# Optimization experiments

Measured on AMD Instinct MI355X. Metric: run time of the kernel, lower is better.

## Reference

```python
import jax, jax.numpy as jnp
import numpy as np

B, S, D = 4, 2048, 1024
H = 16
HD = D // H  # head dim = 64


def setup_inputs() -> dict:
    key = jax.random.key(0)
    ks = jax.random.split(key, 9)
    s = 1.0 / np.sqrt(D)
    return {
        "Q": jax.random.normal(ks[0], (B, S, D), dtype=jnp.float32),
        "K": jax.random.normal(ks[1], (B, S, D), dtype=jnp.float32),
        "V": jax.random.normal(ks[2], (B, S, D), dtype=jnp.float32),
        "Wq": jax.random.uniform(ks[3], (D, D), jnp.float32, -s, s),
        "bq": jax.random.uniform(ks[4], (D,), jnp.float32, -s, s),
        "Wk": jax.random.uniform(ks[5], (D, D), jnp.float32, -s, s),
        "bk": jax.random.uniform(ks[6], (D,), jnp.float32, -s, s),
        "Wv": jax.random.uniform(ks[7], (D, D), jnp.float32, -s, s),
        "bv": jax.random.uniform(ks[8], (D,), jnp.float32, -s, s),
    }


def reference(Q, K, V, Wq, bq, Wk, bk, Wv, bv):
    # Linear projections, split into heads: (B, H, S, HD)
    def proj(x, W, b):
        y = x @ W + b  # torch Linear uses x @ W.T; here W is stored pre-transposed (D_in, D_out)
        return y.reshape(B, S, H, HD).transpose(0, 2, 1, 3)

    q = proj(Q, Wq, bq)
    k = proj(K, Wk, bk)
    v = proj(V, Wv, bv)

    scale = 1.0 / jnp.sqrt(jnp.float32(HD))
    scores = jnp.einsum("bhqd,bhkd->bhqk", q, k) * scale  # (B,H,S,S)
    # causal mask (mask=True path): -inf above the diagonal
    causal = jnp.triu(jnp.full((S, S), -jnp.inf, dtype=scores.dtype), k=1)
    scores = scores + causal
    attn = jax.nn.softmax(scores, axis=-1)
    ctx = jnp.einsum("bhqk,bhkd->bhqd", attn, v)  # (B,H,S,HD)
    return ctx.transpose(0, 2, 1, 3).reshape(B, S, H * HD)
```

## Files before the change

kernel.cpp:

```cpp
#include <hip/hip_runtime.h>
#include <hip/hip_bf16.h>
#include <stdint.h>

#define B_  4
#define S_  2048
#define D_  1024
#define H_  16
#define HD_ 64
#define LOG2E 1.44269504088896f

typedef unsigned short u16;
typedef short bf16x8 __attribute__((ext_vector_type(8)));
typedef float f32x4 __attribute__((ext_vector_type(4)));

static __device__ __forceinline__ u16 f2bf(float f) {
    union { float f; uint32_t u; } v; v.f = f;
    return (u16)((v.u + 0x7FFF + ((v.u >> 16) & 1)) >> 16);
}

static __device__ __forceinline__ uint32_t cvt_pk_bf16(float lo, float hi) {
    uint32_t r;
    asm("v_cvt_pk_bf16_f32 %0, %1, %2" : "=v"(r) : "v"(lo), "v"(hi));
    return r;
}

static __device__ __forceinline__ uint32_t pk2(float lo, float hi) {
    return __builtin_amdgcn_perm(__float_as_uint(hi), __float_as_uint(lo), 0x07060302u);
}

static __device__ __forceinline__ bf16x8 rd_swz(const u16* base, int row, int slot) {
    return *(const bf16x8*)((const char*)base + row * 128 + ((slot ^ (row & 7)) << 4));
}

static __device__ __forceinline__ void gll_swz(const u16* grow0, size_t stride,
                                               u16* lds_chunk, int lane) {
    const int r = lane >> 3;
    const int slot = (lane & 7) ^ r;
    const u16* g = grow0 + (size_t)r * stride + slot * 8;
    __builtin_amdgcn_global_load_lds(
        (const __attribute__((address_space(1))) uint32_t*)g,
        (__attribute__((address_space(3))) uint32_t*)lds_chunk, 16, 0, 0);
}

__global__ __launch_bounds__(256) void wtrans(
    const float* __restrict__ W0, const float* __restrict__ W1, const float* __restrict__ W2,
    u16* __restrict__ T0, u16* __restrict__ T1, u16* __restrict__ T2)
{
    const float* W = blockIdx.z == 0 ? W0 : (blockIdx.z == 1 ? W1 : W2);
    u16* T       = blockIdx.z == 0 ? T0 : (blockIdx.z == 1 ? T1 : T2);
    __shared__ float t[32][33];
    const int n0 = blockIdx.x * 32, k0 = blockIdx.y * 32;
    const int tx = threadIdx.x, ty = threadIdx.y;
#pragma unroll
    for (int i = 0; i < 4; ++i)
        t[ty + i * 8][tx] = W[(size_t)(k0 + ty + i * 8) * D_ + n0 + tx];
    __syncthreads();
#pragma unroll
    for (int i = 0; i < 4; ++i)
        T[(size_t)(n0 + ty + i * 8) * D_ + k0 + tx] = f2bf(t[tx][ty + i * 8]);
}

template <int MODE>
__global__ __launch_bounds__(256) void proj_gemm(
    const float* __restrict__ X, const u16* __restrict__ Wt,
    const float* __restrict__ bias, u16* __restrict__ out)
{
    __shared__ __align__(16) u16 lA[2][128 * 64];
    __shared__ __align__(16) u16 lB[2][128 * 64];
    const int tid = threadIdx.x;
    const int m0 = blockIdx.x * 128, n0 = blockIdx.y * 128;
    const int w = tid >> 6, lane = tid & 63;
    const int lr = lane & 15, lg = lane >> 4;
    const int wr = (w >> 1) * 64, wc = (w & 1) * 64;

    f32x4 acc[4][4] = {};
    float4 areg[8];

    auto loadA = [&](int k0) {
#pragma unroll
        for (int i = 0; i < 8; ++i) {
            const int lin = i * 1024 + tid * 4;
            const int r = lin >> 6, c = lin & 63;
            areg[i] = *(const float4*)(X + (size_t)(m0 + r) * D_ + k0 + c);
        }
    };
    auto writeA = [&](u16* dst) {
#pragma unroll
        for (int i = 0; i < 8; ++i) {
            const int lin = i * 1024 + tid * 4;
            const int r = lin >> 6, c = lin & 63;
            uint2 pk;
            pk.x = pk2(areg[i].x, areg[i].y);
            pk.y = pk2(areg[i].z, areg[i].w);
            const int phys = r * 128 + (((c >> 3) ^ (r & 7)) << 4) + ((c & 7) << 1);
            *(uint2*)((char*)dst + phys) = pk;
        }
    };
    auto stageB = [&](int k0, u16* dst) {
#pragma unroll
        for (int i = 0; i < 4; ++i) {
            const int c = w * 4 + i;
            gll_swz(Wt + (size_t)(n0 + c * 8) * D_ + k0, D_, dst + c * 512, lane);
        }
    };
    auto mfmaStep = [&](const u16* A, const u16* Bb) {
#pragma unroll
        for (int kk = 0; kk < 2; ++kk) {
            bf16x8 af[4], bfr[4];
#pragma unroll
            for (int m = 0; m < 4; ++m)
                af[m] = rd_swz(A, wr + m * 16 + lr, kk * 4 + lg);
#pragma unroll
            for (int n = 0; n < 4; ++n)
                bfr[n] = rd_swz(Bb, wc + n * 16 + lr, kk * 4 + lg);
#pragma unroll
            for (int m = 0; m < 4; ++m)
#pragma unroll
                for (int n = 0; n < 4; ++n)
                    acc[m][n] = __builtin_amdgcn_mfma_f32_16x16x32_bf16(af[m], bfr[n], acc[m][n], 0, 0, 0);
        }
    };

    loadA(0);
    stageB(0, lB[0]);
    writeA(lA[0]);
    __syncthreads();

    for (int k0 = 0, s = 0; k0 < D_; k0 += 64, s ^= 1) {
        const int nk = k0 + 64;
        if (nk < D_) {
            loadA(nk);
            stageB(nk, lB[s ^ 1]);
        }
        mfmaStep(lA[s], lB[s]);
        if (nk < D_) writeA(lA[s ^ 1]);
        __syncthreads();
    }

#pragma unroll
    for (int m = 0; m < 4; ++m)
#pragma unroll
        for (int n = 0; n < 4; ++n)
#pragma unroll
            for (int j = 0; j < 4; ++j) {
                const int gm = m0 + wr + m * 16 + lg * 4 + j;
                const int gn = n0 + wc + n * 16 + lr;
                float y = acc[m][n][j] + bias[gn];
                if (MODE == 0) y *= 0.125f * LOG2E;
                const int bb = gm >> 11, s2 = gm & (S_ - 1);
                const int h = gn >> 6, hd = gn & 63;
                size_t off;
                if (MODE < 2) off = (((size_t)bb * H_ + h) * S_ + s2) * HD_ + hd;
                else {
                    const int s6 = s2 & 63;
                    const int sp = (s2 & ~63) | (s6 & 0x20) | ((s6 & 0xC) << 1) |
                                   ((s6 & 0x10) >> 2) | (s6 & 3);
                    off = (((size_t)bb * H_ + h) * HD_ + hd) * S_ + sp;
                }
                out[off] = f2bf(y);
            }
}

__global__ __launch_bounds__(512) void attn_kernel(
    const u16* __restrict__ qb, const u16* __restrict__ kb,
    const u16* __restrict__ vtb, float* __restrict__ out)
{
    const int bx = blockIdx.x;
    const int bh = bx & 63;
    const int pi = bx >> 6;
    const int b = bh >> 4, h = bh & 15;
    const int tid = threadIdx.x;
    const int w = tid >> 6, lane = tid & 63;
    const int lr = lane & 15, lg = lane >> 4;

    __shared__ __align__(16) u16 lds[2][4][64 * 64];

    const size_t kbase = (size_t)bh * S_ * HD_;
    const size_t vbase = (size_t)bh * HD_ * S_;

    union { uint32_t u[4]; bf16x8 v; } onesf;
    onesf.u[0] = onesf.u[1] = onesf.u[2] = onesf.u[3] = 0x3F803F80u;

    for (int e = 0; e < 2; ++e) {
        const int qi = e ? (7 - pi) : pi;
        const int q0 = qi * 256;
        const int qrb = q0 + w * 32;

        bf16x8 qf0[2], qf1[2];
#pragma unroll
        for (int s = 0; s < 2; ++s) {
            const size_t qoff = ((size_t)bh * S_ + qrb + s * 16 + lr) * HD_;
            qf0[s] = *(const bf16x8*)(qb + qoff + lg * 8);
            qf1[s] = *(const bf16x8*)(qb + qoff + 32 + lg * 8);
        }

        f32x4 oacc[2][4] = {};
        f32x4 lacc[2] = {};
        const int tmax = 4 * qi + 3;

        auto stage = [&](int tp, int set) {
            const int kvA = tp * 64, kvB = kvA + 64;
            u16* d = &lds[set][0][0];
            gll_swz(kb + kbase + (size_t)(kvA + w * 8) * HD_, HD_, d + w * 512, lane);
            gll_swz(vtb + vbase + (size_t)(w * 8) * S_ + kvA, S_, d + 4096 + w * 512, lane);
            gll_swz(kb + kbase + (size_t)(kvB + w * 8) * HD_, HD_, d + 8192 + w * 512, lane);
            gll_swz(vtb + vbase + (size_t)(w * 8) * S_ + kvB, S_, d + 12288 + w * 512, lane);
        };

        auto compute = [&](int t, const u16* lK, const u16* lV) {
            const int kv0 = t * 64;
            if (kv0 > qrb + 31) return;
            const bool a0 = (kv0 <= qrb + 15);

            f32x4 sacc[2][4];
            __builtin_amdgcn_s_setprio(1);
#pragma unroll
            for (int n = 0; n < 4; ++n) {
                const bf16x8 k0f = rd_swz(lK, n * 16 + lr, lg);
                const bf16x8 k1f = rd_swz(lK, n * 16 + lr, 4 + lg);
                f32x4 z1 = {};
                z1 = __builtin_amdgcn_mfma_f32_16x16x32_bf16(k0f, qf0[1], z1, 0, 0, 0);
                z1 = __builtin_amdgcn_mfma_f32_16x16x32_bf16(k1f, qf1[1], z1, 0, 0, 0);
                sacc[1][n] = z1;
                if (a0) {
                    f32x4 z0 = {};
                    z0 = __builtin_amdgcn_mfma_f32_16x16x32_bf16(k0f, qf0[0], z0, 0, 0, 0);
                    z0 = __builtin_amdgcn_mfma_f32_16x16x32_bf16(k1f, qf1[0], z0, 0, 0, 0);
                    sacc[0][n] = z0;
                }
            }
            __builtin_amdgcn_s_setprio(0);

            if (t >= tmax - 3) {
#pragma unroll
                for (int s = 0; s < 2; ++s)
#pragma unroll
                    for (int n = 0; n < 4; ++n)
#pragma unroll
                        for (int j = 0; j < 4; ++j)
                            if (kv0 + n * 16 + lg * 4 + j > qrb + s * 16 + lr)
                                sacc[s][n][j] = -1e30f;
            }

            union { uint32_t u[4]; bf16x8 v; } pa[2][2];
#pragma unroll
            for (int s = 0; s < 2; ++s) {
                if (s == 0 && !a0) continue;
                uint32_t pw[4][2];
#pragma unroll
                for (int n = 0; n < 4; ++n)
#pragma unroll
                    for (int jh = 0; jh < 2; ++jh)
                        pw[n][jh] = cvt_pk_bf16(exp2f(sacc[s][n][2 * jh]),
                                                exp2f(sacc[s][n][2 * jh + 1]));
                pa[s][0].u[0] = pw[0][0]; pa[s][0].u[1] = pw[0][1];
                pa[s][0].u[2] = pw[1][0]; pa[s][0].u[3] = pw[1][1];
                pa[s][1].u[0] = pw[2][0]; pa[s][1].u[1] = pw[2][1];
                pa[s][1].u[2] = pw[3][0]; pa[s][1].u[3] = pw[3][1];
            }

            __builtin_amdgcn_s_setprio(1);
#pragma unroll
            for (int n = 0; n < 4; ++n) {
                const int row = n * 16 + lr;
                const bf16x8 vf0 = rd_swz(lV, row, lg);
                const bf16x8 vf1 = rd_swz(lV, row, 4 + lg);
                oacc[1][n] = __builtin_amdgcn_mfma_f32_16x16x32_bf16(pa[1][0].v, vf0, oacc[1][n], 0, 0, 0);
                oacc[1][n] = __builtin_amdgcn_mfma_f32_16x16x32_bf16(pa[1][1].v, vf1, oacc[1][n], 0, 0, 0);
                if (a0) {
                    oacc[0][n] = __builtin_amdgcn_mfma_f32_16x16x32_bf16(pa[0][0].v, vf0, oacc[0][n], 0, 0, 0);
                    oacc[0][n] = __builtin_amdgcn_mfma_f32_16x16x32_bf16(pa[0][1].v, vf1, oacc[0][n], 0, 0, 0);
                }
            }
            lacc[1] = __builtin_amdgcn_mfma_f32_16x16x32_bf16(pa[1][0].v, onesf.v, lacc[1], 0, 0, 0);
            lacc[1] = __builtin_amdgcn_mfma_f32_16x16x32_bf16(pa[1][1].v, onesf.v, lacc[1], 0, 0, 0);
            if (a0) {
                lacc[0] = __builtin_amdgcn_mfma_f32_16x16x32_bf16(pa[0][0].v, onesf.v, lacc[0], 0, 0, 0);
                lacc[0] = __builtin_amdgcn_mfma_f32_16x16x32_bf16(pa[0][1].v, onesf.v, lacc[0], 0, 0, 0);
            }
            __builtin_amdgcn_s_setprio(0);
        };

        stage(0, 0);
        __syncthreads();

        for (int tp = 0, st = 0; tp <= tmax; tp += 2, st ^= 1) {
            if (tp + 2 <= tmax) stage(tp + 2, st ^ 1);
            const u16* d = &lds[st][0][0];
            compute(tp, d, d + 4096);
            compute(tp + 1, d + 8192, d + 12288);
            __syncthreads();
        }

#pragma unroll
        for (int s = 0; s < 2; ++s) {
            f32x4 inv;
#pragma unroll
            for (int j = 0; j < 4; ++j) inv[j] = 1.f / lacc[s][j];
#pragma unroll
            for (int j = 0; j < 4; ++j) {
                const int row = q0 + w * 32 + s * 16 + lg * 4 + j;
#pragma unroll
                for (int n = 0; n < 4; ++n)
                    out[((size_t)b * S_ + row) * D_ + h * HD_ + n * 16 + lr] = oacc[s][n][j] * inv[j];
            }
        }
    }
}

extern "C" void kernel_launch(void* const* d_in, const int* in_sizes, int n_in,
                              void* d_out, int out_size, void* d_ws, size_t ws_size,
                              hipStream_t stream) {
    const float* Q  = (const float*)d_in[0];
    const float* K  = (const float*)d_in[1];
    const float* V  = (const float*)d_in[2];
    const float* Wq = (const float*)d_in[3];
    const float* bq = (const float*)d_in[4];
    const float* Wk = (const float*)d_in[5];
    const float* bk = (const float*)d_in[6];
    const float* Wv = (const float*)d_in[7];
    const float* bv = (const float*)d_in[8];
    float* out = (float*)d_out;

    char* ws = (char*)d_ws;
    const size_t WT_BYTES  = (size_t)D_ * D_ * 2;
    const size_t QKV_BYTES = (size_t)B_ * S_ * D_ * 2;
    u16* Wtq = (u16*)(ws);
    u16* Wtk = (u16*)(ws + WT_BYTES);
    u16* Wtv = (u16*)(ws + 2 * WT_BYTES);
    u16* qb  = (u16*)(ws + 3 * WT_BYTES);
    u16* kb  = (u16*)(ws + 3 * WT_BYTES + QKV_BYTES);
    u16* vtb = (u16*)(ws + 3 * WT_BYTES + 2 * QKV_BYTES);

    wtrans<<<dim3(32, 32, 3), dim3(32, 8), 0, stream>>>(Wq, Wk, Wv, Wtq, Wtk, Wtv);
    proj_gemm<0><<<dim3(64, 8), dim3(256), 0, stream>>>(Q, Wtq, bq, qb);
    proj_gemm<1><<<dim3(64, 8), dim3(256), 0, stream>>>(K, Wtk, bk, kb);
    proj_gemm<2><<<dim3(64, 8), dim3(256), 0, stream>>>(V, Wtv, bv, vtb);
    attn_kernel<<<dim3(256), dim3(512), 0, stream>>>(qb, kb, vtb, out);
}
```

Measured before the change: 151.6 us.

## Split attention into 1024 smaller blocks with permuted causal tile scheduling

Attention work is redistributed from 256 blocks of 512 threads, each handling a paired 256-row query tile, to 1024 blocks of 256 threads, each handling one 128-row query tile. A permutation table mixes long and short causal tiles across each group of block indices. The double-buffered LDS staging is replaced by a single 32 KB buffer with two barriers per iteration, so K/V loads are no longer overlapped with compute. The aim is better occupancy and load balance across CUs, at the cost of losing that prefetch overlap.

```diff
diff --git a/kernel.cpp b/kernel.cpp
--- a/kernel.cpp
+++ b/kernel.cpp
@@ -161,19 +161,21 @@
             }
 }
 
-__global__ __launch_bounds__(512) void attn_kernel(
+__global__ __launch_bounds__(256) void attn_kernel(
     const u16* __restrict__ qb, const u16* __restrict__ kb,
     const u16* __restrict__ vtb, float* __restrict__ out)
 {
-    const int bx = blockIdx.x;
-    const int bh = bx & 63;
-    const int pi = bx >> 6;
+    const int bid = blockIdx.x;
+    const int slot = bid & 255, round = bid >> 8;
+    const int s15 = slot & 15;
+    const int qi = (int)((0x4B3C691E5A2D780FULL >> (((s15 ^ round) & 15) * 4)) & 15);
+    const int bh = (round << 4) | (slot >> 4);
     const int b = bh >> 4, h = bh & 15;
     const int tid = threadIdx.x;
     const int w = tid >> 6, lane = tid & 63;
     const int lr = lane & 15, lg = lane >> 4;
 
-    __shared__ __align__(16) u16 lds[2][4][64 * 64];
+    __shared__ __align__(16) u16 lds4[4][64 * 64];
 
     const size_t kbase = (size_t)bh * S_ * HD_;
     const size_t vbase = (size_t)bh * HD_ * S_;
@@ -181,129 +183,123 @@
     union { uint32_t u[4]; bf16x8 v; } onesf;
     onesf.u[0] = onesf.u[1] = onesf.u[2] = onesf.u[3] = 0x3F803F80u;
 
-    for (int e = 0; e < 2; ++e) {
-        const int qi = e ? (7 - pi) : pi;
-        const int q0 = qi * 256;
-        const int qrb = q0 + w * 32;
-
-        bf16x8 qf0[2], qf1[2];
+    const int q0 = qi * 128;
+    const int qrb = q0 + w * 32;
+
+    bf16x8 qf0[2], qf1[2];
+#pragma unroll
+    for (int s = 0; s < 2; ++s) {
+        const size_t qoff = ((size_t)bh * S_ + qrb + s * 16 + lr) * HD_;
+        qf0[s] = *(const bf16x8*)(qb + qoff + lg * 8);
+        qf1[s] = *(const bf16x8*)(qb + qoff + 32 + lg * 8);
+    }
+
+    f32x4 oacc[2][4] = {};
+    f32x4 lacc[2] = {};
+    const int tmax = 2 * qi + 1;
+
+    auto compute = [&](int t, const u16* lK, const u16* lV) {
+        const int kv0 = t * 64;
+        if (kv0 > qrb + 31) return;
+        const bool a0 = (kv0 <= qrb + 15);
+
+        f32x4 sacc[2][4];
+        __builtin_amdgcn_s_setprio(1);
+#pragma unroll
+        for (int n = 0; n < 4; ++n) {
+            const bf16x8 k0f = rd_swz(lK, n * 16 + lr, lg);
+            const bf16x8 k1f = rd_swz(lK, n * 16 + lr, 4 + lg);
+            f32x4 z1 = {};
+            z1 = __builtin_amdgcn_mfma_f32_16x16x32_bf16(k0f, qf0[1], z1, 0, 0, 0);
+            z1 = __builtin_amdgcn_mfma_f32_16x16x32_bf16(k1f, qf1[1], z1, 0, 0, 0);
+            sacc[1][n] = z1;
+            if (a0) {
+                f32x4 z0 = {};
+                z0 = __builtin_amdgcn_mfma_f32_16x16x32_bf16(k0f, qf0[0], z0, 0, 0, 0);
+                z0 = __builtin_amdgcn_mfma_f32_16x16x32_bf16(k1f, qf1[0], z0, 0, 0, 0);
+                sacc[0][n] = z0;
+            }
+        }
+        __builtin_amdgcn_s_setprio(0);
+
+        if (t >= tmax - 1) {
+#pragma unroll
+            for (int s = 0; s < 2; ++s)
+#pragma unroll
+                for (int n = 0; n < 4; ++n)
+#pragma unroll
+                    for (int j = 0; j < 4; ++j)
+                        if (kv0 + n * 16 + lg * 4 + j > qrb + s * 16 + lr)
+                            sacc[s][n][j] = -1e30f;
+        }
+
+        union { uint32_t u[4]; bf16x8 v; } pa[2][2];
 #pragma unroll
         for (int s = 0; s < 2; ++s) {
-            const size_t qoff = ((size_t)bh * S_ + qrb + s * 16 + lr) * HD_;
-            qf0[s] = *(const bf16x8*)(qb + qoff + lg * 8);
-            qf1[s] = *(const bf16x8*)(qb + qoff + 32 + lg * 8);
-        }
-
-        f32x4 oacc[2][4] = {};
-        f32x4 lacc[2] = {};
-        const int tmax = 4 * qi + 3;
-
-        auto stage = [&](int tp, int set) {
-            const int kvA = tp * 64, kvB = kvA + 64;
-            u16* d = &lds[set][0][0];
-            gll_swz(kb + kbase + (size_t)(kvA + w * 8) * HD_, HD_, d + w * 512, lane);
-            gll_swz(vtb + vbase + (size_t)(w * 8) * S_ + kvA, S_, d + 4096 + w * 512, lane);
-            gll_swz(kb + kbase + (size_t)(kvB + w * 8) * HD_, HD_, d + 8192 + w * 512, lane);
-            gll_swz(vtb + vbase + (size_t)(w * 8) * S_ + kvB, S_, d + 12288 + w * 512, lane);
-        };
-
-        auto compute = [&](int t, const u16* lK, const u16* lV) {
-            const int kv0 = t * 64;
-            if (kv0 > qrb + 31) return;
-            const bool a0 = (kv0 <= qrb + 15);
-
-            f32x4 sacc[2][4];
-            __builtin_amdgcn_s_setprio(1);
-#pragma unroll
-            for (int n = 0; n < 4; ++n) {
-                const bf16x8 k0f = rd_swz(lK, n * 16 + lr, lg);
-                const bf16x8 k1f = rd_swz(lK, n * 16 + lr, 4 + lg);
-                f32x4 z1 = {};
-                z1 = __builtin_amdgcn_mfma_f32_16x16x32_bf16(k0f, qf0[1], z1, 0, 0, 0);
-                z1 = __builtin_amdgcn_mfma_f32_16x16x32_bf16(k1f, qf1[1], z1, 0, 0, 0);
-                sacc[1][n] = z1;
-                if (a0) {
-                    f32x4 z0 = {};
-                    z0 = __builtin_amdgcn_mfma_f32_16x16x32_bf16(k0f, qf0[0], z0, 0, 0, 0);
-                    z0 = __builtin_amdgcn_mfma_f32_16x16x32_bf16(k1f, qf1[0], z0, 0, 0, 0);
-                    sacc[0][n] = z0;
-                }
+            if (s == 0 && !a0) continue;
+            uint32_t pw[4][2];
+#pragma unroll
+            for (int n = 0; n < 4; ++n)
+#pragma unroll
+                for (int jh = 0; jh < 2; ++jh)
+                    pw[n][jh] = cvt_pk_bf16(exp2f(sacc[s][n][2 * jh]),
+                                            exp2f(sacc[s][n][2 * jh + 1]));
+            pa[s][0].u[0] = pw[0][0]; pa[s][0].u[1] = pw[0][1];
+            pa[s][0].u[2] = pw[1][0]; pa[s][0].u[3] = pw[1][1];
+            pa[s][1].u[0] = pw[2][0]; pa[s][1].u[1] = pw[2][1];
+            pa[s][1].u[2] = pw[3][0]; pa[s][1].u[3] = pw[3][1];
+        }
+
+        __builtin_amdgcn_s_setprio(1);
+#pragma unroll
+        for (int n = 0; n < 4; ++n) {
+            const int row = n * 16 + lr;
+            const bf16x8 vf0 = rd_swz(lV, row, lg);
+            const bf16x8 vf1 = rd_swz(lV, row, 4 + lg);
+            oacc[1][n] = __builtin_amdgcn_mfma_f32_16x16x32_bf16(pa[1][0].v, vf0, oacc[1][n], 0, 0, 0);
+            oacc[1][n] = __builtin_amdgcn_mfma_f32_16x16x32_bf16(pa[1][1].v, vf1, oacc[1][n], 0, 0, 0);
+            if (a0) {
+                oacc[0][n] = __builtin_amdgcn_mfma_f32_16x16x32_bf16(pa[0][0].v, vf0, oacc[0][n], 0, 0, 0);
+                oacc[0][n] = __builtin_amdgcn_mfma_f32_16x16x32_bf16(pa[0][1].v, vf1, oacc[0][n], 0, 0, 0);
             }
-            __builtin_amdgcn_s_setprio(0);
-
-            if (t >= tmax - 3) {
-#pragma unroll
-                for (int s = 0; s < 2; ++s)
-#pragma unroll
-                    for (int n = 0; n < 4; ++n)
-#pragma unroll
-                        for (int j = 0; j < 4; ++j)
-                            if (kv0 + n * 16 + lg * 4 + j > qrb + s * 16 + lr)
-                                sacc[s][n][j] = -1e30f;
-            }
-
-            union { uint32_t u[4]; bf16x8 v; } pa[2][2];
-#pragma unroll
-            for (int s = 0; s < 2; ++s) {
-                if (s == 0 && !a0) continue;
-                uint32_t pw[4][2];
-#pragma unroll
-                for (int n = 0; n < 4; ++n)
-#pragma unroll
-                    for (int jh = 0; jh < 2; ++jh)
-                        pw[n][jh] = cvt_pk_bf16(exp2f(sacc[s][n][2 * jh]),
-                                                exp2f(sacc[s][n][2 * jh + 1]));
-                pa[s][0].u[0] = pw[0][0]; pa[s][0].u[1] = pw[0][1];
-                pa[s][0].u[2] = pw[1][0]; pa[s][0].u[3] = pw[1][1];
-                pa[s][1].u[0] = pw[2][0]; pa[s][1].u[1] = pw[2][1];
-                pa[s][1].u[2] = pw[3][0]; pa[s][1].u[3] = pw[3][1];
-            }
-
-            __builtin_amdgcn_s_setprio(1);
-#pragma unroll
-            for (int n = 0; n < 4; ++n) {
-                const int row = n * 16 + lr;
-                const bf16x8 vf0 = rd_swz(lV, row, lg);
-                const bf16x8 vf1 = rd_swz(lV, row, 4 + lg);
-                oacc[1][n] = __builtin_amdgcn_mfma_f32_16x16x32_bf16(pa[1][0].v, vf0, oacc[1][n], 0, 0, 0);
-                oacc[1][n] = __builtin_amdgcn_mfma_f32_16x16x32_bf16(pa[1][1].v, vf1, oacc[1][n], 0, 0, 0);
-                if (a0) {
-                    oacc[0][n] = __builtin_amdgcn_mfma_f32_16x16x32_bf16(pa[0][0].v, vf0, oacc[0][n], 0, 0, 0);
-                    oacc[0][n] = __builtin_amdgcn_mfma_f32_16x16x32_bf16(pa[0][1].v, vf1, oacc[0][n], 0, 0, 0);
-                }
-            }
-            lacc[1] = __builtin_amdgcn_mfma_f32_16x16x32_bf16(pa[1][0].v, onesf.v, lacc[1], 0, 0, 0);
-            lacc[1] = __builtin_amdgcn_mfma_f32_16x16x32_bf16(pa[1][1].v, onesf.v, lacc[1], 0, 0, 0);
-            if (a0) {
-                lacc[0] = __builtin_amdgcn_mfma_f32_16x16x32_bf16(pa[0][0].v, onesf.v, lacc[0], 0, 0, 0);
-                lacc[0] = __builtin_amdgcn_mfma_f32_16x16x32_bf16(pa[0][1].v, onesf.v, lacc[0], 0, 0, 0);
-            }
-            __builtin_amdgcn_s_setprio(0);
-        };
-
-        stage(0, 0);
+        }
+        lacc[1] = __builtin_amdgcn_mfma_f32_16x16x32_bf16(pa[1][0].v, onesf.v, lacc[1], 0, 0, 0);
+        lacc[1] = __builtin_amdgcn_mfma_f32_16x16x32_bf16(pa[1][1].v, onesf.v, lacc[1], 0, 0, 0);
+        if (a0) {
+            lacc[0] = __builtin_amdgcn_mfma_f32_16x16x32_bf16(pa[0][0].v, onesf.v, lacc[0], 0, 0, 0);
+            lacc[0] = __builtin_amdgcn_mfma_f32_16x16x32_bf16(pa[0][1].v, onesf.v, lacc[0], 0, 0, 0);
+        }
+        __builtin_amdgcn_s_setprio(0);
+    };
+
+    for (int tp = 0; tp <= tmax; tp += 2) {
+        const int kvA = tp * 64, kvB = kvA + 64;
         __syncthreads();
-
-        for (int tp = 0, st = 0; tp <= tmax; tp += 2, st ^= 1) {
-            if (tp + 2 <= tmax) stage(tp + 2, st ^ 1);
-            const u16* d = &lds[st][0][0];
-            compute(tp, d, d + 4096);
-            compute(tp + 1, d + 8192, d + 12288);
-            __syncthreads();
-        }
-
-#pragma unroll
-        for (int s = 0; s < 2; ++s) {
-            f32x4 inv;
-#pragma unroll
-            for (int j = 0; j < 4; ++j) inv[j] = 1.f / lacc[s][j];
-#pragma unroll
-            for (int j = 0; j < 4; ++j) {
-                const int row = q0 + w * 32 + s * 16 + lg * 4 + j;
-#pragma unroll
-                for (int n = 0; n < 4; ++n)
-                    out[((size_t)b * S_ + row) * D_ + h * HD_ + n * 16 + lr] = oacc[s][n][j] * inv[j];
-            }
+#pragma unroll
+        for (int u = 0; u < 2; ++u) {
+            const int rr = (2 * w + u) * 8;
+            gll_swz(kb + kbase + (size_t)(kvA + rr) * HD_, HD_, &lds4[0][rr * 64], lane);
+            gll_swz(vtb + vbase + (size_t)rr * S_ + kvA, S_, &lds4[1][rr * 64], lane);
+            gll_swz(kb + kbase + (size_t)(kvB + rr) * HD_, HD_, &lds4[2][rr * 64], lane);
+            gll_swz(vtb + vbase + (size_t)rr * S_ + kvB, S_, &lds4[3][rr * 64], lane);
+        }
+        __syncthreads();
+
+        compute(tp, lds4[0], lds4[1]);
+        compute(tp + 1, lds4[2], lds4[3]);
+    }
+
+#pragma unroll
+    for (int s = 0; s < 2; ++s) {
+        f32x4 inv;
+#pragma unroll
+        for (int j = 0; j < 4; ++j) inv[j] = 1.f / lacc[s][j];
+#pragma unroll
+        for (int j = 0; j < 4; ++j) {
+            const int row = q0 + w * 32 + s * 16 + lg * 4 + j;
+#pragma unroll
+            for (int n = 0; n < 4; ++n)
+                out[((size_t)b * S_ + row) * D_ + h * HD_ + n * 16 + lr] = oacc[s][n][j] * inv[j];
         }
     }
 }
@@ -336,5 +332,5 @@
     proj_gemm<0><<<dim3(64, 8), dim3(256), 0, stream>>>(Q, Wtq, bq, qb);
     proj_gemm<1><<<dim3(64, 8), dim3(256), 0, stream>>>(K, Wtk, bk, kb);
     proj_gemm<2><<<dim3(64, 8), dim3(256), 0, stream>>>(V, Wtv, bv, vtb);
-    attn_kernel<<<dim3(256), dim3(512), 0, stream>>>(qb, kb, vtb, out);
-}
+    attn_kernel<<<dim3(1024), dim3(256), 0, stream>>>(qb, kb, vtb, out);
+}
```

After: 161.6 us. 1.07x slower.
